# Optimization experiments

Measured on AMD Instinct MI355X. Metric: run time of the kernel, lower is better.

Reference implementation:

```python
import jax, jax.numpy as jnp
import numpy as np

B, S, D, H = 2, 2048, 1024, 16
HD = D // H
EPS = 1e-5


def setup_inputs() -> dict:
    key = jax.random.key(0)
    ks = jax.random.split(key, 8)
    std = 1.0 / np.sqrt(D)
    x = jax.random.normal(ks[0], (B, S, D), dtype=jnp.float32)
    # causal mask: True = attend (masked_fill where mask==0)
    attention_mask = jnp.tril(jnp.ones((S, S), dtype=bool))[None, None].repeat(B, axis=0)
    return {
        "x": x,
        "attention_mask": attention_mask,
        "ln_gamma": jnp.ones((D,), jnp.float32),
        "ln_beta": jnp.zeros((D,), jnp.float32),
        "w_qkv": jax.random.uniform(ks[1], (D, 3 * D), jnp.float32, -std, std),
        "b_qkv": jnp.zeros((3 * D,), jnp.float32),
        "w_gate": jax.random.uniform(ks[2], (D, D), jnp.float32, -std, std),
        "b_gate": jnp.zeros((D,), jnp.float32),
        "w_out": jax.random.uniform(ks[3], (D, D), jnp.float32, -std, std),
        "b_out": jnp.zeros((D,), jnp.float32),
        "rel_pos_bias": jnp.zeros((1, H, 1, 1), jnp.float32),
    }


def reference(x, attention_mask, ln_gamma, ln_beta, w_qkv, b_qkv,
              w_gate, b_gate, w_out, b_out, rel_pos_bias):
    # LayerNorm over model dim
    mu = jnp.mean(x, axis=-1, keepdims=True)
    var = jnp.mean(jnp.square(x - mu), axis=-1, keepdims=True)
    xn = (x - mu) * jax.lax.rsqrt(var + EPS) * ln_gamma + ln_beta

    qkv = xn @ w_qkv + b_qkv                      # [B,S,3D]
    qkv = qkv.reshape(B, S, 3, H, HD)
    q = qkv[:, :, 0].transpose(0, 2, 1, 3)        # [B,H,S,HD]
    k = qkv[:, :, 1].transpose(0, 2, 1, 3)
    v = qkv[:, :, 2].transpose(0, 2, 1, 3)

    u = jax.nn.silu(xn @ w_gate + b_gate)         # [B,S,D] SiLU gate

    scale = HD ** -0.5
    scores = jnp.einsum('bhqd,bhkd->bhqk', q * scale, k) + rel_pos_bias
    # masked_fill(mask==0, -inf) then sigmoid == zero out masked entries
    attn = jnp.where(attention_mask, jax.nn.sigmoid(scores), 0.0)
    ctx = jnp.einsum('bhqk,bhkd->bhqd', attn, v)  # [B,H,S,HD]
    ctx = ctx.transpose(0, 2, 1, 3).reshape(B, S, D)

    out = (ctx * u) @ w_out + b_out               # gated output proj
    return x + out                                # dropout=eval identity
```

## Files before the change

kernel.cpp:

```cpp
#include <hip/hip_runtime.h>
#include <hip/hip_bf16.h>
#include <cmath>

#define BB 2
#define SS 2048
#define DD 1024
#define HH 16
#define EPS 1e-5f
#define LOG2E 1.44269504088896f
#define QSCALE (0.125f * LOG2E)

typedef __attribute__((ext_vector_type(8))) short short8;
typedef __attribute__((ext_vector_type(4))) float f32x4;

__device__ inline unsigned short f2bf(float f) {
  union { float f; unsigned int u; } v; v.f = f;
  unsigned int u = v.u;
  unsigned int r = (u + 0x7FFFu + ((u >> 16) & 1u)) >> 16;
  return (unsigned short)r;
}
__device__ inline float bf2f(unsigned short h) {
  union { unsigned int u; float f; } v; v.u = ((unsigned int)h) << 16;
  return v.f;
}
__device__ inline unsigned short f2bf_fast(float f) {
  union { float f; unsigned int u; } v; v.f = f;
  return (unsigned short)((v.u + 0x8000u) >> 16);
}

__global__ __launch_bounds__(256) void ln_kernel(
    const float* __restrict__ x, const float* __restrict__ gamma,
    const float* __restrict__ beta, unsigned short* __restrict__ xn) {
  int row = blockIdx.x;
  int t = threadIdx.x;
  const float* xr = x + (size_t)row * DD;
  float4 v = *(const float4*)(xr + t * 4);
  float s = v.x + v.y + v.z + v.w;
  float sq = v.x * v.x + v.y * v.y + v.z * v.z + v.w * v.w;
  for (int off = 32; off > 0; off >>= 1) {
    s += __shfl_down(s, off, 64);
    sq += __shfl_down(sq, off, 64);
  }
  __shared__ float ls[4], lq[4];
  int wave = t >> 6, lane = t & 63;
  if (lane == 0) { ls[wave] = s; lq[wave] = sq; }
  __syncthreads();
  float tot = ls[0] + ls[1] + ls[2] + ls[3];
  float totq = lq[0] + lq[1] + lq[2] + lq[3];
  float mu = tot * (1.0f / DD);
  float var = totq * (1.0f / DD) - mu * mu;
  float rstd = rsqrtf(var + EPS);
  float4 g = *(const float4*)(gamma + t * 4);
  float4 bt = *(const float4*)(beta + t * 4);
  ushort4 o;
  o.x = f2bf((v.x - mu) * rstd * g.x + bt.x);
  o.y = f2bf((v.y - mu) * rstd * g.y + bt.y);
  o.z = f2bf((v.z - mu) * rstd * g.z + bt.z);
  o.w = f2bf((v.w - mu) * rstd * g.w + bt.w);
  *(ushort4*)(xn + (size_t)row * DD + t * 4) = o;
}

__global__ __launch_bounds__(256) void wtrans_all(
    const float* __restrict__ wq, const float* __restrict__ wg,
    const float* __restrict__ wo, unsigned short* __restrict__ wcatT,
    unsigned short* __restrict__ woutT) {
  __shared__ unsigned short tile[32][33];
  int bx = blockIdx.x;
  const float* W;
  unsigned short* Wt;
  int N, colbase;
  if (bx < 96)       { W = wq; Wt = wcatT; N = 3072; colbase = bx * 32; }
  else if (bx < 128) { W = wg; Wt = wcatT + (size_t)3072 * 1024; N = 1024; colbase = (bx - 96) * 32; }
  else               { W = wo; Wt = woutT; N = 1024; colbase = (bx - 128) * 32; }
  int by = blockIdx.y * 32;
  int tx = threadIdx.x & 31, ty = threadIdx.x >> 5;
#pragma unroll
  for (int i = 0; i < 32; i += 8)
    tile[ty + i][tx] = f2bf(W[(size_t)(by + ty + i) * N + colbase + tx]);
  __syncthreads();
#pragma unroll
  for (int i = 0; i < 32; i += 8)
    Wt[(size_t)(colbase + ty + i) * 1024 + by + tx] = tile[tx][ty + i];
}

__global__ __launch_bounds__(256) void gemm_qkvg(
    const unsigned short* __restrict__ A, const unsigned short* __restrict__ Bt,
    const float* __restrict__ bqkv, const float* __restrict__ bgate,
    unsigned short* __restrict__ qkb, unsigned short* __restrict__ vTb,
    unsigned short* __restrict__ ub) {
  __shared__ unsigned short SH[128 * 64];
  unsigned short* As = SH;
  unsigned short* Bs = SH + 128 * 32;
  const int K = 1024;
  int tid = threadIdx.x;
  int wave = tid >> 6, lane = tid & 63;
  int quad = lane >> 4, m16 = lane & 15;
  int wm = wave >> 1, wn = wave & 1;
  int m0 = blockIdx.y * 128, n0 = blockIdx.x * 128;

  int lrow = tid >> 2;
  int lcol = (tid & 3) * 8;
  const unsigned short* Ar0 = A + (size_t)(m0 + lrow) * K + lcol;
  const unsigned short* Ar1 = A + (size_t)(m0 + lrow + 64) * K + lcol;
  const unsigned short* Br0 = Bt + (size_t)(n0 + lrow) * K + lcol;
  const unsigned short* Br1 = Bt + (size_t)(n0 + lrow + 64) * K + lcol;

  f32x4 acc[4][4];
#pragma unroll
  for (int i = 0; i < 4; ++i)
#pragma unroll
    for (int j = 0; j < 4; ++j) acc[i][j] = (f32x4){0.f, 0.f, 0.f, 0.f};

  uint4 a0 = *(const uint4*)Ar0;
  uint4 a1 = *(const uint4*)Ar1;
  uint4 b0 = *(const uint4*)Br0;
  uint4 b1 = *(const uint4*)Br1;

  for (int k0 = 0; k0 < K; k0 += 32) {
    __syncthreads();
    *(uint4*)&As[lrow * 32 + lcol] = a0;
    *(uint4*)&As[(lrow + 64) * 32 + lcol] = a1;
    *(uint4*)&Bs[lrow * 32 + lcol] = b0;
    *(uint4*)&Bs[(lrow + 64) * 32 + lcol] = b1;
    __syncthreads();
    if (k0 + 32 < K) {
      a0 = *(const uint4*)(Ar0 + k0 + 32);
      a1 = *(const uint4*)(Ar1 + k0 + 32);
      b0 = *(const uint4*)(Br0 + k0 + 32);
      b1 = *(const uint4*)(Br1 + k0 + 32);
    }
    short8 af[4], bfr[4];
#pragma unroll
    for (int mi = 0; mi < 4; ++mi)
      af[mi] = *(const short8*)&As[(wm * 64 + mi * 16 + m16) * 32 + quad * 8];
#pragma unroll
    for (int ni = 0; ni < 4; ++ni)
      bfr[ni] = *(const short8*)&Bs[(wn * 64 + ni * 16 + m16) * 32 + quad * 8];
#pragma unroll
    for (int mi = 0; mi < 4; ++mi)
#pragma unroll
      for (int ni = 0; ni < 4; ++ni)
        acc[mi][ni] = __builtin_amdgcn_mfma_f32_16x16x32_bf16(
            af[mi], bfr[ni], acc[mi][ni], 0, 0, 0);
  }

  int sec = n0 >> 10;
  if (sec == 2) {
    int bat = m0 >> 11;
    int s_base = m0 & 2047;
    int dgbase = n0 - 2048;
#pragma unroll
    for (int p = 0; p < 2; ++p) {
      __syncthreads();
      if (wn == p) {
#pragma unroll
        for (int ni = 0; ni < 4; ++ni) {
          int dl = ni * 16 + m16;
          float bb = bqkv[2048 + dgbase + p * 64 + dl];
#pragma unroll
          for (int mi = 0; mi < 4; ++mi)
#pragma unroll
            for (int r = 0; r < 4; ++r) {
              int sl = wm * 64 + mi * 16 + quad * 4 + r;
              int sls = sl ^ ((dl & 7) << 4);
              SH[dl * 128 + sls] = f2bf(acc[mi][ni][r] + bb);
            }
        }
      }
      __syncthreads();
      int dl = tid >> 2;
      int dg = dgbase + p * 64 + dl;
      unsigned short* dst =
          vTb + ((size_t)(bat * 16 + (dg >> 6)) * 64 + (dg & 63)) * 2048 + s_base;
#pragma unroll
      for (int i = 0; i < 4; ++i) {
        int s0 = (tid & 3) * 8 + i * 32;
        int s0s = s0 ^ ((dl & 7) << 4);
        *(uint4*)(dst + s0) = *(const uint4*)&SH[dl * 128 + s0s];
      }
    }
  } else {
    int nwin = n0 + wn * 64;
    if (sec <= 1) {
      float qs = (sec == 0) ? QSCALE : 1.0f;
#pragma unroll
      for (int ni = 0; ni < 4; ++ni) {
        int col = nwin + ni * 16 + m16;
        float bb = bqkv[col];
#pragma unroll
        for (int mi = 0; mi < 4; ++mi)
#pragma unroll
          for (int r = 0; r < 4; ++r) {
            int row = m0 + wm * 64 + mi * 16 + quad * 4 + r;
            qkb[(size_t)row * 2048 + col] = f2bf((acc[mi][ni][r] + bb) * qs);
          }
      }
    } else {
#pragma unroll
      for (int ni = 0; ni < 4; ++ni) {
        int col = nwin + ni * 16 + m16;
        int g = col - 3072;
        float bb = bgate[g];
#pragma unroll
        for (int mi = 0; mi < 4; ++mi)
#pragma unroll
          for (int r = 0; r < 4; ++r) {
            int row = m0 + wm * 64 + mi * 16 + quad * 4 + r;
            float v = acc[mi][ni][r] + bb;
            v = v * __builtin_amdgcn_rcpf(1.0f + exp2f(-v * LOG2E));
            ub[(size_t)row * 1024 + g] = f2bf(v);
          }
      }
    }
  }
}

__global__ __launch_bounds__(256) void gemm_out(
    const unsigned short* __restrict__ A, const unsigned short* __restrict__ Bt,
    const float* __restrict__ bias, const float* __restrict__ resid,
    float* __restrict__ C) {
  __shared__ unsigned short As[128 * 32];
  __shared__ unsigned short Bs[128 * 32];
  const int K = 1024, N = 1024;
  int tid = threadIdx.x;
  int wave = tid >> 6, lane = tid & 63;
  int quad = lane >> 4, m16 = lane & 15;
  int wm = wave >> 1, wn = wave & 1;
  int m0 = blockIdx.y * 128, n0 = blockIdx.x * 128;
  int lrow = tid >> 2;
  int lcol = (tid & 3) * 8;
  const unsigned short* Ar0 = A + (size_t)(m0 + lrow) * K + lcol;
  const unsigned short* Ar1 = A + (size_t)(m0 + lrow + 64) * K + lcol;
  const unsigned short* Br0 = Bt + (size_t)(n0 + lrow) * K + lcol;
  const unsigned short* Br1 = Bt + (size_t)(n0 + lrow + 64) * K + lcol;

  f32x4 acc[4][4];
#pragma unroll
  for (int i = 0; i < 4; ++i)
#pragma unroll
    for (int j = 0; j < 4; ++j) acc[i][j] = (f32x4){0.f, 0.f, 0.f, 0.f};

  uint4 a0 = *(const uint4*)Ar0;
  uint4 a1 = *(const uint4*)Ar1;
  uint4 b0 = *(const uint4*)Br0;
  uint4 b1 = *(const uint4*)Br1;

  for (int k0 = 0; k0 < K; k0 += 32) {
    __syncthreads();
    *(uint4*)&As[lrow * 32 + lcol] = a0;
    *(uint4*)&As[(lrow + 64) * 32 + lcol] = a1;
    *(uint4*)&Bs[lrow * 32 + lcol] = b0;
    *(uint4*)&Bs[(lrow + 64) * 32 + lcol] = b1;
    __syncthreads();
    if (k0 + 32 < K) {
      a0 = *(const uint4*)(Ar0 + k0 + 32);
      a1 = *(const uint4*)(Ar1 + k0 + 32);
      b0 = *(const uint4*)(Br0 + k0 + 32);
      b1 = *(const uint4*)(Br1 + k0 + 32);
    }
    short8 af[4], bfr[4];
#pragma unroll
    for (int mi = 0; mi < 4; ++mi)
      af[mi] = *(const short8*)&As[(wm * 64 + mi * 16 + m16) * 32 + quad * 8];
#pragma unroll
    for (int ni = 0; ni < 4; ++ni)
      bfr[ni] = *(const short8*)&Bs[(wn * 64 + ni * 16 + m16) * 32 + quad * 8];
#pragma unroll
    for (int mi = 0; mi < 4; ++mi)
#pragma unroll
      for (int ni = 0; ni < 4; ++ni)
        acc[mi][ni] = __builtin_amdgcn_mfma_f32_16x16x32_bf16(
            af[mi], bfr[ni], acc[mi][ni], 0, 0, 0);
  }
#pragma unroll
  for (int ni = 0; ni < 4; ++ni) {
    int col = n0 + wn * 64 + ni * 16 + m16;
    float bb = bias[col];
#pragma unroll
    for (int mi = 0; mi < 4; ++mi)
#pragma unroll
      for (int r = 0; r < 4; ++r) {
        int row = m0 + wm * 64 + mi * 16 + quad * 4 + r;
        C[(size_t)row * N + col] =
            acc[mi][ni][r] + bb + resid[(size_t)row * N + col];
      }
  }
}

__global__ __launch_bounds__(256) void attn_mfma(
    const unsigned short* __restrict__ qk, const unsigned short* __restrict__ vT,
    const unsigned short* __restrict__ u, const float* __restrict__ rpb,
    unsigned short* __restrict__ prod) {
  __shared__ unsigned short Ks[64 * 72];
  __shared__ unsigned short Vs[64 * 72];
  __shared__ unsigned short Ps[64 * 72];

  int qtA = blockIdx.x;
  int qtB = 31 - qtA;
  int q0A = qtA * 64, q0B = qtB * 64;
  int bh = blockIdx.y;
  int b = bh >> 4, h = bh & 15;
  int t = threadIdx.x;
  int wave = t >> 6, lane = t & 63;
  int quad = lane >> 4, m16 = lane & 15;

  const unsigned short* qbase = qk + (size_t)(b * SS) * 2048 + h * 64;
  const unsigned short* kbase = qbase + 1024;
  const unsigned short* vbase = vT + (size_t)bh * 64 * 2048;

  int row = t >> 3, blk8 = (t & 7) * 8;

  short8 qfA[2], qfB[2];
#pragma unroll
  for (int s = 0; s < 2; ++s) {
    qfA[s] = *(const short8*)(qbase + (size_t)(q0A + wave * 16 + m16) * 2048 + s * 32 + quad * 8);
    qfB[s] = *(const short8*)(qbase + (size_t)(q0B + wave * 16 + m16) * 2048 + s * 32 + quad * 8);
  }

  f32x4 zero4 = {0.f, 0.f, 0.f, 0.f};
  f32x4 caccA[4], caccB[4];
#pragma unroll
  for (int nb = 0; nb < 4; ++nb) { caccA[nb] = zero4; caccB[nb] = zero4; }

  float hb2 = rpb[h] * LOG2E;
  float cexp = exp2f(-hb2);
  int ktmax = qtB;
  int psw = quad << 3;
  int psr = ((m16 >> 2) & 3) << 3;

  uint4 kv0, kv1, vv0, vv1;
  {
    const unsigned short* kp = kbase + (size_t)row * 2048 + blk8;
    const unsigned short* vp = vbase + (size_t)row * 2048 + blk8;
    kv0 = *(const uint4*)kp;
    kv1 = *(const uint4*)(kp + (size_t)32 * 2048);
    vv0 = *(const uint4*)vp;
    vv1 = *(const uint4*)(vp + (size_t)32 * 2048);
  }

  for (int kt = 0; kt <= ktmax; ++kt) {
    int k0 = kt * 64;
    __syncthreads();
    *(uint4*)&Ks[row * 72 + blk8] = kv0;
    *(uint4*)&Ks[(row + 32) * 72 + blk8] = kv1;
    *(uint4*)&Vs[row * 72 + blk8] = vv0;
    *(uint4*)&Vs[(row + 32) * 72 + blk8] = vv1;
    __syncthreads();
    if (kt < ktmax) {
      int k0n = k0 + 64;
      const unsigned short* kp = kbase + (size_t)(k0n + row) * 2048 + blk8;
      const unsigned short* vp = vbase + (size_t)row * 2048 + k0n + blk8;
      kv0 = *(const uint4*)kp;
      kv1 = *(const uint4*)(kp + (size_t)32 * 2048);
      vv0 = *(const uint4*)vp;
      vv1 = *(const uint4*)(vp + (size_t)32 * 2048);
    }

#pragma unroll
    for (int tile = 0; tile < 2; ++tile) {
      if (tile == 1 && kt > qtA) break;
      const short8* qf = (tile == 0) ? qfB : qfA;
      int q0 = (tile == 0) ? q0B : q0A;
      bool diag = (tile == 0) ? (kt == qtB) : (kt == qtA);
      f32x4* cacc = (tile == 0) ? caccB : caccA;

      f32x4 sacc[4];
#pragma unroll
      for (int nb = 0; nb < 4; ++nb) sacc[nb] = zero4;
#pragma unroll
      for (int s = 0; s < 2; ++s) {
#pragma unroll
        for (int nb = 0; nb < 4; ++nb) {
          short8 bf = *(const short8*)&Ks[(nb * 16 + m16) * 72 + s * 32 + quad * 8];
          sacc[nb] = __builtin_amdgcn_mfma_f32_16x16x32_bf16(qf[s], bf, sacc[nb], 0, 0, 0);
        }
      }
#pragma unroll
      for (int nb = 0; nb < 4; ++nb) {
#pragma unroll
        for (int r = 0; r < 4; ++r) {
          float e = exp2f(-sacc[nb][r]);
          float p = __builtin_amdgcn_rcpf(fmaf(cexp, e, 1.0f));
          if (diag) {
            int key = k0 + nb * 16 + m16;
            int q = q0 + wave * 16 + quad * 4 + r;
            if (key > q) p = 0.f;
          }
          int colS = (nb * 16 + m16) ^ psw;
          Ps[(wave * 16 + quad * 4 + r) * 72 + colS] = f2bf_fast(p);
        }
      }
#pragma unroll
      for (int s = 0; s < 2; ++s) {
        int pcol = (s * 32 + quad * 8) ^ psr;
        short8 a = *(const short8*)&Ps[(wave * 16 + m16) * 72 + pcol];
#pragma unroll
        for (int nb = 0; nb < 4; ++nb) {
          short8 bf = *(const short8*)&Vs[(nb * 16 + m16) * 72 + s * 32 + quad * 8];
          cacc[nb] = __builtin_amdgcn_mfma_f32_16x16x32_bf16(a, bf, cacc[nb], 0, 0, 0);
        }
      }
    }
  }

  const unsigned short* ub_ = u + (size_t)(b * SS) * 1024 + h * 64;
  unsigned short* pb_ = prod + (size_t)(b * SS) * 1024 + h * 64;
#pragma unroll
  for (int nb = 0; nb < 4; ++nb) {
    int d = nb * 16 + m16;
#pragma unroll
    for (int r = 0; r < 4; ++r) {
      int qA = q0A + wave * 16 + quad * 4 + r;
      int qB = q0B + wave * 16 + quad * 4 + r;
      pb_[(size_t)qA * 1024 + d] = f2bf(caccA[nb][r] * bf2f(ub_[(size_t)qA * 1024 + d]));
      pb_[(size_t)qB * 1024 + d] = f2bf(caccB[nb][r] * bf2f(ub_[(size_t)qB * 1024 + d]));
    }
  }
}

extern "C" void kernel_launch(void* const* d_in, const int* in_sizes, int n_in,
                              void* d_out, int out_size, void* d_ws, size_t ws_size,
                              hipStream_t stream) {
  const float* x      = (const float*)d_in[0];
  const float* gamma  = (const float*)d_in[2];
  const float* beta   = (const float*)d_in[3];
  const float* w_qkv  = (const float*)d_in[4];
  const float* b_qkv  = (const float*)d_in[5];
  const float* w_gate = (const float*)d_in[6];
  const float* b_gate = (const float*)d_in[7];
  const float* w_out  = (const float*)d_in[8];
  const float* b_out  = (const float*)d_in[9];
  const float* rpb    = (const float*)d_in[10];
  float* out = (float*)d_out;

  unsigned short* xnb   = (unsigned short*)d_ws;
  unsigned short* qkb   = xnb + 4194304;
  unsigned short* vTb   = qkb + 8388608;
  unsigned short* ub    = vTb + 4194304;
  unsigned short* prodb = ub + 4194304;
  unsigned short* wcatT = prodb + 4194304;
  unsigned short* woutT = wcatT + 4194304;

  ln_kernel<<<BB * SS, 256, 0, stream>>>(x, gamma, beta, xnb);
  wtrans_all<<<dim3(160, 32), 256, 0, stream>>>(w_qkv, w_gate, w_out, wcatT, woutT);
  gemm_qkvg<<<dim3(4096 / 128, 4096 / 128), 256, 0, stream>>>(
      xnb, wcatT, b_qkv, b_gate, qkb, vTb, ub);
  attn_mfma<<<dim3(16, BB * HH), 256, 0, stream>>>(qkb, vTb, ub, rpb, prodb);
  gemm_out<<<dim3(1024 / 128, 4096 / 128), 256, 0, stream>>>(
      prodb, woutT, b_out, x, out);
}
```

Baseline: 245.1 us.

## Split attention key range across two blocks and combine partial contexts

The attention kernel now launches a third grid dimension of two, and each block handles alternating key tiles (even or odd) and writes unnormalized partial context to its own buffer. A new combine kernel sums the two partials, applies the SiLU gate, and writes the product for the output GEMM. This doubles the number of attention blocks from 512 so the GPU's compute units are better filled. The cost is an extra kernel launch, two extra bf16 buffers of global traffic, and an extra bf16 rounding on each partial sum. Because attention is sigmoid-based with no softmax normalization, the partials can simply be added.

Result: no change. 249.7 us (+1.9%).

```diff
diff --git a/kernel.cpp b/kernel.cpp
--- a/kernel.cpp
+++ b/kernel.cpp
@@ -289,8 +289,8 @@
 
 __global__ __launch_bounds__(256) void attn_mfma(
     const unsigned short* __restrict__ qk, const unsigned short* __restrict__ vT,
-    const unsigned short* __restrict__ u, const float* __restrict__ rpb,
-    unsigned short* __restrict__ prod) {
+    const float* __restrict__ rpb,
+    unsigned short* __restrict__ ctx0, unsigned short* __restrict__ ctx1) {
   __shared__ unsigned short Ks[64 * 72];
   __shared__ unsigned short Vs[64 * 72];
   __shared__ unsigned short Ps[64 * 72];
@@ -299,6 +299,7 @@
   int qtB = 31 - qtA;
   int q0A = qtA * 64, q0B = qtB * 64;
   int bh = blockIdx.y;
+  int sk = blockIdx.z;
   int b = bh >> 4, h = bh & 15;
   int t = threadIdx.x;
   int wave = t >> 6, lane = t & 63;
@@ -330,15 +331,16 @@
 
   uint4 kv0, kv1, vv0, vv1;
   {
-    const unsigned short* kp = kbase + (size_t)row * 2048 + blk8;
-    const unsigned short* vp = vbase + (size_t)row * 2048 + blk8;
+    int k00 = sk * 64;
+    const unsigned short* kp = kbase + (size_t)(k00 + row) * 2048 + blk8;
+    const unsigned short* vp = vbase + (size_t)row * 2048 + k00 + blk8;
     kv0 = *(const uint4*)kp;
     kv1 = *(const uint4*)(kp + (size_t)32 * 2048);
     vv0 = *(const uint4*)vp;
     vv1 = *(const uint4*)(vp + (size_t)32 * 2048);
   }
 
-  for (int kt = 0; kt <= ktmax; ++kt) {
+  for (int kt = sk; kt <= ktmax; kt += 2) {
     int k0 = kt * 64;
     __syncthreads();
     *(uint4*)&Ks[row * 72 + blk8] = kv0;
@@ -346,8 +348,8 @@
     *(uint4*)&Vs[row * 72 + blk8] = vv0;
     *(uint4*)&Vs[(row + 32) * 72 + blk8] = vv1;
     __syncthreads();
-    if (kt < ktmax) {
-      int k0n = k0 + 64;
+    if (kt + 2 <= ktmax) {
+      int k0n = k0 + 128;
       const unsigned short* kp = kbase + (size_t)(k0n + row) * 2048 + blk8;
       const unsigned short* vp = vbase + (size_t)row * 2048 + k0n + blk8;
       kv0 = *(const uint4*)kp;
@@ -403,8 +405,8 @@
     }
   }
 
-  const unsigned short* ub_ = u + (size_t)(b * SS) * 1024 + h * 64;
-  unsigned short* pb_ = prod + (size_t)(b * SS) * 1024 + h * 64;
+  unsigned short* cp = (sk == 0) ? ctx0 : ctx1;
+  unsigned short* cp_ = cp + (size_t)(b * SS) * 1024 + h * 64;
 #pragma unroll
   for (int nb = 0; nb < 4; ++nb) {
     int d = nb * 16 + m16;
@@ -412,10 +414,28 @@
     for (int r = 0; r < 4; ++r) {
       int qA = q0A + wave * 16 + quad * 4 + r;
       int qB = q0B + wave * 16 + quad * 4 + r;
-      pb_[(size_t)qA * 1024 + d] = f2bf(caccA[nb][r] * bf2f(ub_[(size_t)qA * 1024 + d]));
-      pb_[(size_t)qB * 1024 + d] = f2bf(caccB[nb][r] * bf2f(ub_[(size_t)qB * 1024 + d]));
-    }
-  }
+      cp_[(size_t)qA * 1024 + d] = f2bf(caccA[nb][r]);
+      cp_[(size_t)qB * 1024 + d] = f2bf(caccB[nb][r]);
+    }
+  }
+}
+
+__global__ __launch_bounds__(256) void combine_kernel(
+    const unsigned short* __restrict__ c0, const unsigned short* __restrict__ c1,
+    const unsigned short* __restrict__ u, unsigned short* __restrict__ prod) {
+  size_t i = ((size_t)blockIdx.x * 256 + threadIdx.x) * 8;
+  uint4 a = *(const uint4*)(c0 + i);
+  uint4 b = *(const uint4*)(c1 + i);
+  uint4 uu = *(const uint4*)(u + i);
+  const unsigned short* ae = (const unsigned short*)&a;
+  const unsigned short* be = (const unsigned short*)&b;
+  const unsigned short* ue = (const unsigned short*)&uu;
+  uint4 o;
+  unsigned short* oe = (unsigned short*)&o;
+#pragma unroll
+  for (int j = 0; j < 8; ++j)
+    oe[j] = f2bf((bf2f(ae[j]) + bf2f(be[j])) * bf2f(ue[j]));
+  *(uint4*)(prod + i) = o;
 }
 
 extern "C" void kernel_launch(void* const* d_in, const int* in_sizes, int n_in,
@@ -438,14 +458,17 @@
   unsigned short* vTb   = qkb + 8388608;
   unsigned short* ub    = vTb + 4194304;
   unsigned short* prodb = ub + 4194304;
-  unsigned short* wcatT = prodb + 4194304;
+  unsigned short* ctx0b = prodb + 4194304;
+  unsigned short* ctx1b = ctx0b + 4194304;
+  unsigned short* wcatT = ctx1b + 4194304;
   unsigned short* woutT = wcatT + 4194304;
 
   ln_kernel<<<BB * SS, 256, 0, stream>>>(x, gamma, beta, xnb);
   wtrans_all<<<dim3(160, 32), 256, 0, stream>>>(w_qkv, w_gate, w_out, wcatT, woutT);
   gemm_qkvg<<<dim3(4096 / 128, 4096 / 128), 256, 0, stream>>>(
       xnb, wcatT, b_qkv, b_gate, qkb, vTb, ub);
-  attn_mfma<<<dim3(16, BB * HH), 256, 0, stream>>>(qkb, vTb, ub, rpb, prodb);
+  attn_mfma<<<dim3(16, BB * HH, 2), 256, 0, stream>>>(qkb, vTb, rpb, ctx0b, ctx1b);
+  combine_kernel<<<4194304 / (256 * 8), 256, 0, stream>>>(ctx0b, ctx1b, ub, prodb);
   gemm_out<<<dim3(1024 / 128, 4096 / 128), 256, 0, stream>>>(
       prodb, woutT, b_out, x, out);
 }
```
